# Performance work log

Measured on AMD Instinct MI355X. Metric: run time of the kernel, lower is better.

## Reference

```python
import jax, jax.numpy as jnp
import numpy as np

N_POINTS = 131072   # dense point cloud, batch['points'][0]
N_NODES = 2048      # coarse node set, batch['points'][-1]
NEIGHBOR_SEL = 32   # config['neighbor_sel']


def setup_inputs() -> dict:
    key = jax.random.key(0)
    k1, k2 = jax.random.split(key)
    point_cloud = jax.random.normal(k1, (N_POINTS, 3), dtype=jnp.float32)
    nodes = jax.random.normal(k2, (N_NODES, 3), dtype=jnp.float32)
    return {"point_cloud": point_cloud, "nodes": nodes, "neighbor_sel": NEIGHBOR_SEL}


def _knn1(points, nodes):
    # pairwise squared distances [N, M] = |p|^2 - 2 p.n + |n|^2
    d2 = (jnp.sum(points * points, axis=-1, keepdims=True)
          - 2.0 * (points @ nodes.T)
          + jnp.sum(nodes * nodes, axis=-1)[None, :])
    pcd_id = jnp.argmin(d2, axis=1)          # [N] nearest node per point (k=1 knn)
    min_d2 = jnp.min(d2, axis=1)             # [N] nearest squared distance
    return min_d2, pcd_id


def _grouping(pcd_id, n_nodes, k):
    # Replicates grouping_wrapper: for each node, collect the first k point
    # indices (in point order) assigned to it; unfilled slots stay -1.
    n = pcd_id.shape[0]
    order = jnp.argsort(pcd_id, stable=True)          # stable -> preserves point order within a node
    sorted_ids = pcd_id[order]                        # [N] non-decreasing node ids
    starts = jnp.searchsorted(sorted_ids, jnp.arange(n_nodes))  # group start offsets [M]
    rank = jnp.arange(n) - starts[sorted_ids]         # within-group rank of each point
    col = jnp.where(rank < k, rank, k)                # overflow slots routed to scratch column k
    patch = jnp.full((n_nodes, k + 1), -1, dtype=jnp.int32)
    patch = patch.at[sorted_ids, col].set(order.astype(jnp.int32))
    patch = patch[:, :k]                              # drop scratch column
    return jnp.maximum(patch, 0)                      # patch[patch < 0] = 0


def reference(point_cloud, nodes, neighbor_sel):
    min_d2, pcd_id = _knn1(point_cloud, nodes)
    patch = _grouping(pcd_id, nodes.shape[0], neighbor_sel)
    # pcd_id returned as [1, N, 1] matching knn(pc[None], nodes[None], k=1)
    return min_d2, pcd_id[None, :, None], patch[None]
```

## Files before the change

### kernel.cpp

```cpp
#include <hip/hip_runtime.h>
#include <hip/hip_bf16.h>

#define NPTS   131072
#define NNODES 2048
#define KSEL   32

#define TKNN   256
#define PPT    4
#define PPG_K  (TKNN * PPT)
#define NGRP_K (NPTS / PPG_K)
#define NCHUNK 8
#define CHN    (NNODES / NCHUNK)

#define GSZ    512
#define NG     (NPTS / GSZ)

typedef unsigned int uint;
typedef unsigned short u16;
typedef unsigned long long u64;
typedef float f2 __attribute__((ext_vector_type(2)));

__device__ __forceinline__ f2 splat(float s) { return (f2){s, s}; }

__device__ __forceinline__ uint f2ord(float d) {
    uint b = __float_as_uint(d);
    return (b & 0x80000000u) ? ~b : (b | 0x80000000u);
}
__device__ __forceinline__ float ord2f(uint t) {
    uint b = (t & 0x80000000u) ? (t ^ 0x80000000u) : ~t;
    return __uint_as_float(b);
}

__global__ __launch_bounds__(256) void prep_nodes(const float* __restrict__ nodes,
                                                  float4* __restrict__ n4) {
    int i = blockIdx.x * 256 + threadIdx.x;
    float x = nodes[3 * i], y = nodes[3 * i + 1], z = nodes[3 * i + 2];
    float nn = __fadd_rn(__fadd_rn(__fmul_rn(x, x), __fmul_rn(y, y)), __fmul_rn(z, z));
    n4[i] = make_float4(x, y, z, nn);
}

__global__ __launch_bounds__(256) void knn_part(const float* __restrict__ pts,
                                                const float4* __restrict__ n4,
                                                u64* __restrict__ knnres) {
    int bid = blockIdx.x;
    int c   = bid & (NCHUNK - 1);
    int g   = bid >> 3;
    int t   = threadIdx.x;

    f2 pp2[2], nx2[2], ny2[2], nz2[2];
    #pragma unroll
    for (int q = 0; q < 2; ++q) {
        #pragma unroll
        for (int h = 0; h < 2; ++h) {
            int pid = g * PPG_K + (2 * q + h) * TKNN + t;
            float p0 = pts[3 * pid], p1 = pts[3 * pid + 1], p2 = pts[3 * pid + 2];
            float pp = __fadd_rn(__fadd_rn(__fmul_rn(p0, p0), __fmul_rn(p1, p1)),
                                 __fmul_rn(p2, p2));
            pp2[q][h] = pp;
            nx2[q][h] = __fmul_rn(-2.0f, p0);
            ny2[q][h] = __fmul_rn(-2.0f, p1);
            nz2[q][h] = __fmul_rn(-2.0f, p2);
        }
    }

    const float4* np = n4 + c * CHN;
    float best[PPT];
    int   qb[PPT];
    #pragma unroll
    for (int p = 0; p < PPT; ++p) { best[p] = 3.4e38f; qb[p] = 0; }

    #pragma unroll 2
    for (int jj = 0; jj < CHN; jj += 4) {
        float4 v0 = np[jj + 0];
        float4 v1 = np[jj + 1];
        float4 v2 = np[jj + 2];
        float4 v3 = np[jj + 3];

        f2 d[2][4];
        #pragma unroll
        for (int q = 0; q < 2; ++q) {
            {   f2 m = nx2[q] * splat(v0.x);
                f2 r = __builtin_elementwise_fma(ny2[q], splat(v0.y), m);
                r    = __builtin_elementwise_fma(nz2[q], splat(v0.z), r);
                d[q][0] = (pp2[q] + r) + splat(v0.w); }
            {   f2 m = nx2[q] * splat(v1.x);
                f2 r = __builtin_elementwise_fma(ny2[q], splat(v1.y), m);
                r    = __builtin_elementwise_fma(nz2[q], splat(v1.z), r);
                d[q][1] = (pp2[q] + r) + splat(v1.w); }
            {   f2 m = nx2[q] * splat(v2.x);
                f2 r = __builtin_elementwise_fma(ny2[q], splat(v2.y), m);
                r    = __builtin_elementwise_fma(nz2[q], splat(v2.z), r);
                d[q][2] = (pp2[q] + r) + splat(v2.w); }
            {   f2 m = nx2[q] * splat(v3.x);
                f2 r = __builtin_elementwise_fma(ny2[q], splat(v3.y), m);
                r    = __builtin_elementwise_fma(nz2[q], splat(v3.z), r);
                d[q][3] = (pp2[q] + r) + splat(v3.w); }
        }

        #pragma unroll
        for (int p = 0; p < PPT; ++p) {
            int q = p >> 1;
            float e0 = (p & 1) ? d[q][0].y : d[q][0].x;
            float e1 = (p & 1) ? d[q][1].y : d[q][1].x;
            float e2 = (p & 1) ? d[q][2].y : d[q][2].x;
            float e3 = (p & 1) ? d[q][3].y : d[q][3].x;
            float m1 = fminf(fminf(best[p], e0), e1);
            float nb = fminf(fminf(m1, e2), e3);
            qb[p]   = (nb < best[p]) ? jj : qb[p];
            best[p] = nb;
        }
    }

    #pragma unroll
    for (int p = 0; p < PPT; ++p) {
        int q = p >> 1, h = p & 1;
        float nx = nx2[q][h], ny = ny2[q][h], nz = nz2[q][h], pp = pp2[q][h];
        float b  = best[p];
        int base = qb[p];
        float dd[4];
        #pragma unroll
        for (int o = 0; o < 4; ++o) {
            float4 v = np[base + o];
            float m = __fmul_rn(nx, v.x);
            float r = __builtin_fmaf(ny, v.y, m);
            r       = __builtin_fmaf(nz, v.z, r);
            dd[o]   = __fadd_rn(__fadd_rn(pp, r), v.w);
        }
        int off = 3;
        if (dd[2] == b) off = 2;
        if (dd[1] == b) off = 1;
        if (dd[0] == b) off = 0;

        int pid = g * PPG_K + p * TKNN + t;
        u64 key = ((u64)f2ord(b) << 32) | (uint)(c * CHN + base + off);
        atomicMin(&knnres[pid], key);
    }
}

__global__ __launch_bounds__(256) void merge_hist(const u64* __restrict__ knnres,
                                                  float* __restrict__ out_d2,
                                                  float* __restrict__ out_id,
                                                  int* __restrict__ pcd,
                                                  u16* __restrict__ hist16,
                                                  float* __restrict__ patch) {
    __shared__ uint lh[NNODES];
    int g = blockIdx.x, t = threadIdx.x;
    patch[(size_t)g * 256 + t] = 0.0f;
    for (int i = t; i < NNODES; i += 256) lh[i] = 0;
    __syncthreads();

    #pragma unroll
    for (int q = 0; q < GSZ / 256; ++q) {
        int pid = g * GSZ + q * 256 + t;
        u64 key = knnres[pid];
        uint bi = (uint)key;
        float d = ord2f((uint)(key >> 32));
        atomicAdd(&lh[bi], 1u);
        out_d2[pid] = d;
        out_id[pid] = (float)bi;
        pcd[pid]    = (int)bi;
    }
    __syncthreads();
    for (int i = t; i < NNODES; i += 256)
        hist16[(size_t)g * NNODES + i] = (u16)lh[i];
}

__global__ __launch_bounds__(256) void scan_offs(const u16* __restrict__ hist16,
                                                 uint* __restrict__ offs) {
    int t = threadIdx.x, lane = t & 63, wv = t >> 6;
    int node = blockIdx.x * 4 + wv;

    uint v0 = hist16[(size_t)(4 * lane + 0) * NNODES + node];
    uint v1 = hist16[(size_t)(4 * lane + 1) * NNODES + node];
    uint v2 = hist16[(size_t)(4 * lane + 2) * NNODES + node];
    uint v3 = hist16[(size_t)(4 * lane + 3) * NNODES + node];
    uint s = v0 + v1 + v2 + v3;
    uint a = s;
    #pragma unroll
    for (int d = 1; d < 64; d <<= 1) {
        uint y = __shfl_up(a, d, 64);
        if (lane >= d) a += y;
    }
    uint base = a - s;
    uint4 o = make_uint4(base, base + v0, base + v0 + v1, base + v0 + v1 + v2);
    *(uint4*)(offs + (size_t)node * NG + 4 * lane) = o;
}

__global__ __launch_bounds__(256) void scatter_patch(const int* __restrict__ pcd,
                                                     const uint* __restrict__ offs,
                                                     float* __restrict__ patch) {
    __shared__ int ids[GSZ];
    int g = blockIdx.x, t = threadIdx.x;
    ids[t]       = pcd[g * GSZ + t];
    ids[256 + t] = pcd[g * GSZ + 256 + t];
    __syncthreads();

    int i0 = t, i1 = 256 + t;
    int my0 = ids[i0], my1 = ids[i1];
    int r0 = 0, r1 = 0;
    #pragma unroll 8
    for (int j = 0; j < GSZ; ++j) {
        int id = ids[j];
        r0 += (j < i0 && id == my0) ? 1 : 0;
        r1 += (j < i1 && id == my1) ? 1 : 0;
    }
    uint rk0 = offs[(size_t)my0 * NG + g] + (uint)r0;
    uint rk1 = offs[(size_t)my1 * NG + g] + (uint)r1;
    if (rk0 < KSEL) patch[(size_t)my0 * KSEL + rk0] = (float)(g * GSZ + i0);
    if (rk1 < KSEL) patch[(size_t)my1 * KSEL + rk1] = (float)(g * GSZ + i1);
}

extern "C" void kernel_launch(void* const* d_in, const int* in_sizes, int n_in,
                              void* d_out, int out_size, void* d_ws, size_t ws_size,
                              hipStream_t stream) {
    const float* pts   = (const float*)d_in[0];
    const float* nodes = (const float*)d_in[1];

    float* out       = (float*)d_out;
    float* out_d2    = out;
    float* out_id    = out + NPTS;
    float* out_patch = out + 2 * NPTS;

    char* ws = (char*)d_ws;
    u64*   knnres = (u64*) ws;
    u16*   hist16 = (u16*) (ws + (1 << 20));
    uint*  offs   = (uint*) (ws + (2 << 20));
    int*   pcd    = (int*)  (ws + (4 << 20));
    float4* n4    = (float4*)(ws + (4 << 20) + (512 << 10));

    hipMemsetAsync(knnres, 0xFF, (size_t)NPTS * sizeof(u64), stream);
    prep_nodes<<<NNODES / 256, 256, 0, stream>>>(nodes, n4);
    knn_part<<<NGRP_K * NCHUNK, TKNN, 0, stream>>>(pts, n4, knnres);
    merge_hist<<<NG, 256, 0, stream>>>(knnres, out_d2, out_id, pcd, hist16, out_patch);
    scan_offs<<<NNODES / 4, 256, 0, stream>>>(hist16, offs);
    scatter_patch<<<NG, 256, 0, stream>>>(pcd, offs, out_patch);
}
```

Baseline: 120.5 us.

## Fuse histogram, scan and scatter into one cooperative kernel; halve points per thread

```diff
diff --git a/kernel.cpp b/kernel.cpp
--- a/kernel.cpp
+++ b/kernel.cpp
@@ -1,12 +1,15 @@
 #include <hip/hip_runtime.h>
 #include <hip/hip_bf16.h>
+#include <hip/hip_cooperative_groups.h>
+
+namespace cg = cooperative_groups;
 
 #define NPTS   131072
 #define NNODES 2048
 #define KSEL   32
 
 #define TKNN   256
-#define PPT    4
+#define PPT    2
 #define PPG_K  (TKNN * PPT)
 #define NGRP_K (NPTS / PPG_K)
 #define NCHUNK 8
@@ -31,12 +34,16 @@
     return __uint_as_float(b);
 }
 
-__global__ __launch_bounds__(256) void prep_nodes(const float* __restrict__ nodes,
-                                                  float4* __restrict__ n4) {
+__global__ __launch_bounds__(256) void prep_init(const float* __restrict__ nodes,
+                                                 float4* __restrict__ n4,
+                                                 u64* __restrict__ knnres) {
     int i = blockIdx.x * 256 + threadIdx.x;
-    float x = nodes[3 * i], y = nodes[3 * i + 1], z = nodes[3 * i + 2];
-    float nn = __fadd_rn(__fadd_rn(__fmul_rn(x, x), __fmul_rn(y, y)), __fmul_rn(z, z));
-    n4[i] = make_float4(x, y, z, nn);
+    knnres[i] = ~0ull;
+    if (i < NNODES) {
+        float x = nodes[3 * i], y = nodes[3 * i + 1], z = nodes[3 * i + 2];
+        float nn = __fadd_rn(__fadd_rn(__fmul_rn(x, x), __fmul_rn(y, y)), __fmul_rn(z, z));
+        n4[i] = make_float4(x, y, z, nn);
+    }
 }
 
 __global__ __launch_bounds__(256) void knn_part(const float* __restrict__ pts,
@@ -47,20 +54,17 @@
     int g   = bid >> 3;
     int t   = threadIdx.x;
 
-    f2 pp2[2], nx2[2], ny2[2], nz2[2];
-    #pragma unroll
-    for (int q = 0; q < 2; ++q) {
-        #pragma unroll
-        for (int h = 0; h < 2; ++h) {
-            int pid = g * PPG_K + (2 * q + h) * TKNN + t;
-            float p0 = pts[3 * pid], p1 = pts[3 * pid + 1], p2 = pts[3 * pid + 2];
-            float pp = __fadd_rn(__fadd_rn(__fmul_rn(p0, p0), __fmul_rn(p1, p1)),
-                                 __fmul_rn(p2, p2));
-            pp2[q][h] = pp;
-            nx2[q][h] = __fmul_rn(-2.0f, p0);
-            ny2[q][h] = __fmul_rn(-2.0f, p1);
-            nz2[q][h] = __fmul_rn(-2.0f, p2);
-        }
+    f2 pp2, nx2, ny2, nz2;
+    #pragma unroll
+    for (int h = 0; h < 2; ++h) {
+        int pid = g * PPG_K + h * TKNN + t;
+        float p0 = pts[3 * pid], p1 = pts[3 * pid + 1], p2 = pts[3 * pid + 2];
+        float pp = __fadd_rn(__fadd_rn(__fmul_rn(p0, p0), __fmul_rn(p1, p1)),
+                             __fmul_rn(p2, p2));
+        pp2[h] = pp;
+        nx2[h] = __fmul_rn(-2.0f, p0);
+        ny2[h] = __fmul_rn(-2.0f, p1);
+        nz2[h] = __fmul_rn(-2.0f, p2);
     }
 
     const float4* np = n4 + c * CHN;
@@ -69,41 +73,37 @@
     #pragma unroll
     for (int p = 0; p < PPT; ++p) { best[p] = 3.4e38f; qb[p] = 0; }
 
-    #pragma unroll 2
+    #pragma unroll 4
     for (int jj = 0; jj < CHN; jj += 4) {
         float4 v0 = np[jj + 0];
         float4 v1 = np[jj + 1];
         float4 v2 = np[jj + 2];
         float4 v3 = np[jj + 3];
 
-        f2 d[2][4];
-        #pragma unroll
-        for (int q = 0; q < 2; ++q) {
-            {   f2 m = nx2[q] * splat(v0.x);
-                f2 r = __builtin_elementwise_fma(ny2[q], splat(v0.y), m);
-                r    = __builtin_elementwise_fma(nz2[q], splat(v0.z), r);
-                d[q][0] = (pp2[q] + r) + splat(v0.w); }
-            {   f2 m = nx2[q] * splat(v1.x);
-                f2 r = __builtin_elementwise_fma(ny2[q], splat(v1.y), m);
-                r    = __builtin_elementwise_fma(nz2[q], splat(v1.z), r);
-                d[q][1] = (pp2[q] + r) + splat(v1.w); }
-            {   f2 m = nx2[q] * splat(v2.x);
-                f2 r = __builtin_elementwise_fma(ny2[q], splat(v2.y), m);
-                r    = __builtin_elementwise_fma(nz2[q], splat(v2.z), r);
-                d[q][2] = (pp2[q] + r) + splat(v2.w); }
-            {   f2 m = nx2[q] * splat(v3.x);
-                f2 r = __builtin_elementwise_fma(ny2[q], splat(v3.y), m);
-                r    = __builtin_elementwise_fma(nz2[q], splat(v3.z), r);
-                d[q][3] = (pp2[q] + r) + splat(v3.w); }
-        }
+        f2 d0, d1, d2, d3;
+        {   f2 m = nx2 * splat(v0.x);
+            f2 r = __builtin_elementwise_fma(ny2, splat(v0.y), m);
+            r    = __builtin_elementwise_fma(nz2, splat(v0.z), r);
+            d0   = (pp2 + r) + splat(v0.w); }
+        {   f2 m = nx2 * splat(v1.x);
+            f2 r = __builtin_elementwise_fma(ny2, splat(v1.y), m);
+            r    = __builtin_elementwise_fma(nz2, splat(v1.z), r);
+            d1   = (pp2 + r) + splat(v1.w); }
+        {   f2 m = nx2 * splat(v2.x);
+            f2 r = __builtin_elementwise_fma(ny2, splat(v2.y), m);
+            r    = __builtin_elementwise_fma(nz2, splat(v2.z), r);
+            d2   = (pp2 + r) + splat(v2.w); }
+        {   f2 m = nx2 * splat(v3.x);
+            f2 r = __builtin_elementwise_fma(ny2, splat(v3.y), m);
+            r    = __builtin_elementwise_fma(nz2, splat(v3.z), r);
+            d3   = (pp2 + r) + splat(v3.w); }
 
         #pragma unroll
         for (int p = 0; p < PPT; ++p) {
-            int q = p >> 1;
-            float e0 = (p & 1) ? d[q][0].y : d[q][0].x;
-            float e1 = (p & 1) ? d[q][1].y : d[q][1].x;
-            float e2 = (p & 1) ? d[q][2].y : d[q][2].x;
-            float e3 = (p & 1) ? d[q][3].y : d[q][3].x;
+            float e0 = p ? d0.y : d0.x;
+            float e1 = p ? d1.y : d1.x;
+            float e2 = p ? d2.y : d2.x;
+            float e3 = p ? d3.y : d3.x;
             float m1 = fminf(fminf(best[p], e0), e1);
             float nb = fminf(fminf(m1, e2), e3);
             qb[p]   = (nb < best[p]) ? jj : qb[p];
@@ -113,8 +113,7 @@
 
     #pragma unroll
     for (int p = 0; p < PPT; ++p) {
-        int q = p >> 1, h = p & 1;
-        float nx = nx2[q][h], ny = ny2[q][h], nz = nz2[q][h], pp = pp2[q][h];
+        float nx = nx2[p], ny = ny2[p], nz = nz2[p], pp = pp2[p];
         float b  = best[p];
         int base = qb[p];
         float dd[4];
@@ -137,14 +136,17 @@
     }
 }
 
-__global__ __launch_bounds__(256) void merge_hist(const u64* __restrict__ knnres,
+__global__ __launch_bounds__(256) void tail_fused(const u64* __restrict__ knnres,
                                                   float* __restrict__ out_d2,
                                                   float* __restrict__ out_id,
-                                                  int* __restrict__ pcd,
                                                   u16* __restrict__ hist16,
+                                                  uint* __restrict__ offs,
                                                   float* __restrict__ patch) {
+    cg::grid_group grid = cg::this_grid();
     __shared__ uint lh[NNODES];
+    __shared__ int  ids[GSZ];
     int g = blockIdx.x, t = threadIdx.x;
+
     patch[(size_t)g * 256 + t] = 0.0f;
     for (int i = t; i < NNODES; i += 256) lh[i] = 0;
     __syncthreads();
@@ -156,44 +158,37 @@
         uint bi = (uint)key;
         float d = ord2f((uint)(key >> 32));
         atomicAdd(&lh[bi], 1u);
+        ids[q * 256 + t] = (int)bi;
         out_d2[pid] = d;
         out_id[pid] = (float)bi;
-        pcd[pid]    = (int)bi;
     }
     __syncthreads();
     for (int i = t; i < NNODES; i += 256)
         hist16[(size_t)g * NNODES + i] = (u16)lh[i];
-}
-
-__global__ __launch_bounds__(256) void scan_offs(const u16* __restrict__ hist16,
-                                                 uint* __restrict__ offs) {
-    int t = threadIdx.x, lane = t & 63, wv = t >> 6;
-    int node = blockIdx.x * 4 + wv;
-
-    uint v0 = hist16[(size_t)(4 * lane + 0) * NNODES + node];
-    uint v1 = hist16[(size_t)(4 * lane + 1) * NNODES + node];
-    uint v2 = hist16[(size_t)(4 * lane + 2) * NNODES + node];
-    uint v3 = hist16[(size_t)(4 * lane + 3) * NNODES + node];
-    uint s = v0 + v1 + v2 + v3;
-    uint a = s;
-    #pragma unroll
-    for (int d = 1; d < 64; d <<= 1) {
-        uint y = __shfl_up(a, d, 64);
-        if (lane >= d) a += y;
-    }
-    uint base = a - s;
-    uint4 o = make_uint4(base, base + v0, base + v0 + v1, base + v0 + v1 + v2);
-    *(uint4*)(offs + (size_t)node * NG + 4 * lane) = o;
-}
-
-__global__ __launch_bounds__(256) void scatter_patch(const int* __restrict__ pcd,
-                                                     const uint* __restrict__ offs,
-                                                     float* __restrict__ patch) {
-    __shared__ int ids[GSZ];
-    int g = blockIdx.x, t = threadIdx.x;
-    ids[t]       = pcd[g * GSZ + t];
-    ids[256 + t] = pcd[g * GSZ + 256 + t];
-    __syncthreads();
+
+    grid.sync();
+
+    int lane = t & 63, wv = t >> 6;
+    #pragma unroll
+    for (int rep = 0; rep < 2; ++rep) {
+        int node = rep * 1024 + g * 4 + wv;
+        uint v0 = hist16[(size_t)(4 * lane + 0) * NNODES + node];
+        uint v1 = hist16[(size_t)(4 * lane + 1) * NNODES + node];
+        uint v2 = hist16[(size_t)(4 * lane + 2) * NNODES + node];
+        uint v3 = hist16[(size_t)(4 * lane + 3) * NNODES + node];
+        uint s = v0 + v1 + v2 + v3;
+        uint a = s;
+        #pragma unroll
+        for (int d = 1; d < 64; d <<= 1) {
+            uint y = __shfl_up(a, d, 64);
+            if (lane >= d) a += y;
+        }
+        uint base = a - s;
+        uint4 o = make_uint4(base, base + v0, base + v0 + v1, base + v0 + v1 + v2);
+        *(uint4*)(offs + (size_t)node * NG + 4 * lane) = o;
+    }
+
+    grid.sync();
 
     int i0 = t, i1 = 256 + t;
     int my0 = ids[i0], my1 = ids[i1];
@@ -225,13 +220,13 @@
     u64*   knnres = (u64*) ws;
     u16*   hist16 = (u16*) (ws + (1 << 20));
     uint*  offs   = (uint*) (ws + (2 << 20));
-    int*   pcd    = (int*)  (ws + (4 << 20));
-    float4* n4    = (float4*)(ws + (4 << 20) + (512 << 10));
-
-    hipMemsetAsync(knnres, 0xFF, (size_t)NPTS * sizeof(u64), stream);
-    prep_nodes<<<NNODES / 256, 256, 0, stream>>>(nodes, n4);
+    float4* n4    = (float4*)(ws + (4 << 20));
+
+    prep_init<<<NPTS / 256, 256, 0, stream>>>(nodes, n4, knnres);
     knn_part<<<NGRP_K * NCHUNK, TKNN, 0, stream>>>(pts, n4, knnres);
-    merge_hist<<<NG, 256, 0, stream>>>(knnres, out_d2, out_id, pcd, hist16, out_patch);
-    scan_offs<<<NNODES / 4, 256, 0, stream>>>(hist16, offs);
-    scatter_patch<<<NG, 256, 0, stream>>>(pcd, offs, out_patch);
-}
+
+    void* args[] = { (void*)&knnres, (void*)&out_d2, (void*)&out_id,
+                     (void*)&hist16, (void*)&offs, (void*)&out_patch };
+    hipLaunchCooperativeKernel((void*)tail_fused, dim3(NG), dim3(256),
+                               args, 0, stream);
+}
```

New measurement: 180.3 us. 49.6% more time.
